# Kernel optimization log

Hardware: AMD Instinct MI355X
Metric: run time of the kernel (lower is better)

## Reference

```python
import jax, jax.numpy as jnp
import numpy as np

N = 50000      # num nodes
E = 800000     # num edges (no self loops; added in reference like add_remaining_self_loops)
D = 64         # input_dim
H = 128        # hidden_dim
O = 32         # output_dim
EPS = 1.0      # epsilon (privacy)
ALPHA = 0.5
DELTA = 1.0


def setup_inputs() -> dict:
    key = jax.random.key(0)
    ks = jax.random.split(key, 8)
    x = jax.random.normal(ks[0], (N, D), dtype=jnp.float32)
    row = jax.random.randint(ks[1], (E,), 0, N, dtype=jnp.int32)
    off = jax.random.randint(ks[2], (E,), 1, N, dtype=jnp.int32)
    col = (row + off) % N  # guarantees row != col (no pre-existing self loops)
    edge_index = jnp.stack([row, col], axis=0)
    priv_mask = jax.random.bernoulli(ks[3], 0.5, (N,))
    W1 = jax.random.normal(ks[4], (D, H), dtype=jnp.float32) * (1.0 / np.sqrt(D))
    b1 = jnp.zeros((H,), dtype=jnp.float32)
    W2 = jax.random.normal(ks[5], (H, O), dtype=jnp.float32) * (1.0 / np.sqrt(H))
    b2 = jnp.zeros((O,), dtype=jnp.float32)
    return {"x": x, "edge_index": edge_index, "priv_mask": priv_mask,
            "W1": W1, "b1": b1, "W2": W2, "b2": b2}


def _gcn_norm(edge_index, num_nodes, dtype):
    # add_remaining_self_loops + symmetric normalization deg^-1/2[row]*deg^-1/2[col]
    loops = jnp.arange(num_nodes, dtype=edge_index.dtype)
    row = jnp.concatenate([edge_index[0], loops])
    col = jnp.concatenate([edge_index[1], loops])
    deg = jax.ops.segment_sum(jnp.ones(row.shape[0], dtype=dtype), row,
                              num_segments=num_nodes)
    dis = deg ** -0.5  # deg >= 1 thanks to self loops
    norm = dis[row] * dis[col]  # [E+N]
    return row, col, norm


def reference(x, edge_index, priv_mask, W1, b1, W2, b2):
    row, col, norm = _gcn_norm(edge_index, N, x.dtype)
    exp_eps = float(np.exp(EPS))

    # ---- conv1 (GConvDP with per-node bool priv_mask) ----
    x_j = x[row]                                   # [E+N, D] gather
    p = priv_mask[row].astype(x.dtype)[:, None]    # [E+N, 1]
    transformed = ((exp_eps + 1.0) * x_j - 1.0) * (DELTA / (exp_eps - 1.0)) + ALPHA
    msg = norm[:, None] * (p * transformed + (1.0 - p) * x_j)
    h = jax.ops.segment_sum(msg, col, num_segments=N)  # scatter-add aggregate

    h = jax.nn.relu(h @ W1 + b1)
    # F.dropout skipped: reference is deterministic (eval mode)

    # ---- conv2 (called with priv_mask=False, a Python scalar) ----
    # Literal torch semantics: p_j = False -> False*(...) = 0, ~False = -1,
    # so msg = norm * (-x_j).
    msg2 = -norm[:, None] * h[row]                 # [E+N, H]
    h2 = jax.ops.segment_sum(msg2, col, num_segments=N)

    return h2 @ W2 + b2
```

## Files before the change

### kernel.cpp

```cpp
#include <hip/hip_runtime.h>
#include <math.h>

#define C1 2.163953413738653f
#define C0 -0.081976706869326f


typedef __attribute__((ext_vector_type(8))) short bf16x8;
typedef __attribute__((ext_vector_type(4))) float f32x4;

static __device__ __forceinline__ unsigned short f2bf(float f) {
    unsigned b = __float_as_uint(f);
    return (unsigned short)((b + 0x7FFFu + ((b >> 16) & 1u)) >> 16);
}
static __device__ __forceinline__ float bf2f(unsigned short u) {
    return __uint_as_float((unsigned)u << 16);
}

__global__ __launch_bounds__(1024) void k_hist2(const int* __restrict__ row,
                                                const int* __restrict__ col, int E, int chunk,
                                                int* __restrict__ hist,
                                                const float* __restrict__ W1,
                                                const float* __restrict__ W2,
                                                unsigned short* __restrict__ W1b,
                                                unsigned short* __restrict__ W2b) {
    __shared__ int hc[256], hr[256];
    int t = threadIdx.x, b = blockIdx.x;
    if (t < 256) { hc[t] = 0; hr[t] = 0; }
    __syncthreads();
    int lo = b * chunk, hi = min(E, lo + chunk);
    int base = lo + t * 4;
    for (; base + 3 < hi; base += 4096) {
        int4 r4 = *(const int4*)&row[base];
        int4 c4 = *(const int4*)&col[base];
        atomicAdd(&hc[c4.x >> 8], 1); atomicAdd(&hc[c4.y >> 8], 1);
        atomicAdd(&hc[c4.z >> 8], 1); atomicAdd(&hc[c4.w >> 8], 1);
        atomicAdd(&hr[r4.x >> 8], 1); atomicAdd(&hr[r4.y >> 8], 1);
        atomicAdd(&hr[r4.z >> 8], 1); atomicAdd(&hr[r4.w >> 8], 1);
    }
    for (; base < hi; ++base) {
        atomicAdd(&hc[col[base] >> 8], 1);
        atomicAdd(&hr[row[base] >> 8], 1);
    }
    __syncthreads();
    if (t < 256) {
        hist[t * 256 + b] = hc[t];
        hist[65536 + t * 256 + b] = hr[t];
    }
    if (b == 0) {
        for (int i = t; i < 8192; i += 1024) {
            int j = i & 7, l2 = (i >> 3) & 63, kt = (i >> 9) & 1, nt = i >> 10;
            int k = kt * 32 + (l2 >> 4) * 8 + j, n = nt * 16 + (l2 & 15);
            W1b[i] = f2bf(W1[k * 128 + n]);
        }
    } else if (b == 1) {
        for (int i = t; i < 4096; i += 1024) {
            int j = i & 7, l2 = (i >> 3) & 63, kt = (i >> 9) & 3, nt = i >> 11;
            int k = kt * 32 + (l2 >> 4) * 8 + j, n = nt * 16 + (l2 & 15);
            W2b[i] = f2bf(W2[k * 32 + n]);
        }
    }
}

__global__ void k_scan_a(const int* __restrict__ cnt, int* __restrict__ excl,
                         int* __restrict__ bsum, int n) {
    __shared__ int s[256];
    int idx = blockIdx.x * 256 + threadIdx.x;
    int v = (idx < n) ? cnt[idx] : 0;
    s[threadIdx.x] = v;
    __syncthreads();
    for (int off = 1; off < 256; off <<= 1) {
        int t = (threadIdx.x >= off) ? s[threadIdx.x - off] : 0;
        __syncthreads();
        s[threadIdx.x] += t;
        __syncthreads();
    }
    if (idx < n) excl[idx] = s[threadIdx.x] - v;
    if (threadIdx.x == 255) bsum[blockIdx.x] = s[255];
}

__global__ __launch_bounds__(1024) void k_part(const int* __restrict__ row,
                                               const int* __restrict__ col, int E, int chunk,
                                               const int* __restrict__ excl,
                                               const int* __restrict__ bsum,
                                               unsigned* __restrict__ cbuf,
                                               unsigned short* __restrict__ rbuf) {
    __shared__ int sc[512];
    __shared__ int offc[256], offr[256];
    int t = threadIdx.x, b = blockIdx.x;
    if (t < 512) sc[t] = bsum[t];
    __syncthreads();
    int half = t >> 8, d = t & 255;
    for (int off = 1; off < 256; off <<= 1) {
        int u = (t < 512 && d >= off) ? sc[half * 256 + d - off] : 0;
        __syncthreads();
        if (t < 512) sc[t] += u;
        __syncthreads();
    }
    if (t < 256) offc[t] = sc[t] - bsum[t] + excl[t * 256 + b];
    else if (t < 512) offr[d] = sc[t] - bsum[t] + excl[65536 + d * 256 + b];
    __syncthreads();
    int lo = b * chunk, hi = min(E, lo + chunk);
    int base = lo + t * 4;
    for (; base + 3 < hi; base += 4096) {
        int4 r4 = *(const int4*)&row[base];
        int4 c4 = *(const int4*)&col[base];
        int p0 = atomicAdd(&offc[c4.x >> 8], 1);
        cbuf[p0] = ((unsigned)c4.x << 16) | (unsigned)r4.x;
        int p1 = atomicAdd(&offc[c4.y >> 8], 1);
        cbuf[p1] = ((unsigned)c4.y << 16) | (unsigned)r4.y;
        int p2 = atomicAdd(&offc[c4.z >> 8], 1);
        cbuf[p2] = ((unsigned)c4.z << 16) | (unsigned)r4.z;
        int p3 = atomicAdd(&offc[c4.w >> 8], 1);
        cbuf[p3] = ((unsigned)c4.w << 16) | (unsigned)r4.w;
        int q0 = atomicAdd(&offr[r4.x >> 8], 1); rbuf[q0] = (unsigned short)r4.x;
        int q1 = atomicAdd(&offr[r4.y >> 8], 1); rbuf[q1] = (unsigned short)r4.y;
        int q2 = atomicAdd(&offr[r4.z >> 8], 1); rbuf[q2] = (unsigned short)r4.z;
        int q3 = atomicAdd(&offr[r4.w >> 8], 1); rbuf[q3] = (unsigned short)r4.w;
    }
    for (; base < hi; ++base) {
        int r = row[base], c = col[base];
        int pc = atomicAdd(&offc[c >> 8], 1);
        cbuf[pc] = ((unsigned)c << 16) | (unsigned)r;
        int pr = atomicAdd(&offr[r >> 8], 1);
        rbuf[pr] = (unsigned short)r;
    }
}

__global__ __launch_bounds__(256) void k_build(const unsigned short* __restrict__ rbuf,
                                               const unsigned* __restrict__ cbuf,
                                               const int* __restrict__ bsum,
                                               const int* __restrict__ priv,
                                               const float* __restrict__ x, int N, int E, int nbk,
                                               float* __restrict__ dis,
                                               unsigned short* __restrict__ xt,
                                               int* __restrict__ cntC, int* __restrict__ colStart,
                                               unsigned short* __restrict__ eSrc) {
    __shared__ int s1[256], s2[256], s3[256];
    int t = threadIdx.x;
    if ((int)blockIdx.x < nbk) {
        int b = blockIdx.x;
        s1[t] = (t < b) ? bsum[256 + t] : 0;
        __syncthreads();
        for (int off = 128; off > 0; off >>= 1) {
            if (t < off) s1[t] += s1[t + off];
            __syncthreads();
        }
        int rs = s1[0];
        int re = rs + bsum[256 + b];
        __syncthreads();
        s1[t] = 0;
        __syncthreads();
        for (int i = rs + t; i < re; i += 256) atomicAdd(&s1[rbuf[i] & 255], 1);
        __syncthreads();
        int node = b * 256 + t;
        float dv = rsqrtf((float)(s1[t] + 1));
        if (node < N) {
            dis[node] = dv;
            s2[t] = __float_as_int(dv);
            s3[t] = priv[node];
        } else { s2[t] = 0; s3[t] = 0; }
        __syncthreads();
        int base = b * 256;
        for (int i = t; i < 256 * 16; i += 256) {
            int ln = i >> 4;
            int n2 = base + ln;
            if (n2 >= N) continue;
            float d2 = __int_as_float(s2[ln]);
            int p = s3[ln];
            float4 v = ((const float4*)x)[(size_t)n2 * 16 + (i & 15)];
            float4 tr;
            tr.x = p ? fmaf(C1, v.x, C0) : v.x;
            tr.y = p ? fmaf(C1, v.y, C0) : v.y;
            tr.z = p ? fmaf(C1, v.z, C0) : v.z;
            tr.w = p ? fmaf(C1, v.w, C0) : v.w;
            ushort4 o;
            o.x = f2bf(d2 * tr.x); o.y = f2bf(d2 * tr.y);
            o.z = f2bf(d2 * tr.z); o.w = f2bf(d2 * tr.w);
            ((ushort4*)xt)[(size_t)n2 * 16 + (i & 15)] = o;
        }
    } else {
        int b = blockIdx.x - nbk;
        s1[t] = (t < b) ? bsum[t] : 0;
        __syncthreads();
        for (int off = 128; off > 0; off >>= 1) {
            if (t < off) s1[t] += s1[t + off];
            __syncthreads();
        }
        int cs = s1[0];
        int ce = cs + bsum[b];
        __syncthreads();
        s1[t] = 0; s3[t] = 0;
        __syncthreads();
        for (int i = cs + t; i < ce; i += 256) atomicAdd(&s1[(cbuf[i] >> 16) & 255], 1);
        __syncthreads();
        int v = s1[t];
        s2[t] = v;
        __syncthreads();
        for (int off = 1; off < 256; off <<= 1) {
            int u = (t >= off) ? s2[t - off] : 0;
            __syncthreads();
            s2[t] += u;
            __syncthreads();
        }
        int excl = s2[t] - v;
        int c = b * 256 + t;
        if (c < N) { cntC[c] = v; colStart[c] = cs + excl; }
        __syncthreads();
        s2[t] = excl;
        __syncthreads();
        for (int i = cs + t; i < ce; i += 256) {
            unsigned e = cbuf[i];
            int d = (e >> 16) & 255;
            int pos = cs + s2[d] + atomicAdd(&s3[d], 1);
            eSrc[pos] = (unsigned short)(e & 0xFFFFu);
        }
    }
}

__global__ __launch_bounds__(256) void k_gather1(const unsigned short* __restrict__ xt,
                                                 const unsigned short* __restrict__ eSrc,
                                                 const int* __restrict__ colStart,
                                                 const int* __restrict__ cntC,
                                                 const float* __restrict__ dis,
                                                 unsigned short* __restrict__ agg1b, int N) {
    int t = blockIdx.x * blockDim.x + threadIdx.x;
    int c = t >> 6, d = t & 63;
    if (c >= N) return;
    float s = bf2f(xt[(size_t)c * 64 + d]);
    int start = colStart[c], cnt = cntC[c];
    for (int base = 0; base < cnt; base += 64) {
        int m = min(cnt - base, 64);
        int ids = (d < m) ? (int)eSrc[start + base + d] : 0;
        int k = 0;
        for (; k + 8 <= m; k += 8) {
            int r0 = __shfl(ids, k),     r1 = __shfl(ids, k + 1);
            int r2 = __shfl(ids, k + 2), r3 = __shfl(ids, k + 3);
            int r4 = __shfl(ids, k + 4), r5 = __shfl(ids, k + 5);
            int r6 = __shfl(ids, k + 6), r7 = __shfl(ids, k + 7);
            float x0 = bf2f(xt[(size_t)r0 * 64 + d]);
            float x1 = bf2f(xt[(size_t)r1 * 64 + d]);
            float x2 = bf2f(xt[(size_t)r2 * 64 + d]);
            float x3 = bf2f(xt[(size_t)r3 * 64 + d]);
            float x4 = bf2f(xt[(size_t)r4 * 64 + d]);
            float x5 = bf2f(xt[(size_t)r5 * 64 + d]);
            float x6 = bf2f(xt[(size_t)r6 * 64 + d]);
            float x7 = bf2f(xt[(size_t)r7 * 64 + d]);
            s += x0; s += x1; s += x2; s += x3;
            s += x4; s += x5; s += x6; s += x7;
        }
        for (; k + 4 <= m; k += 4) {
            int r0 = __shfl(ids, k),     r1 = __shfl(ids, k + 1);
            int r2 = __shfl(ids, k + 2), r3 = __shfl(ids, k + 3);
            float x0 = bf2f(xt[(size_t)r0 * 64 + d]);
            float x1 = bf2f(xt[(size_t)r1 * 64 + d]);
            float x2 = bf2f(xt[(size_t)r2 * 64 + d]);
            float x3 = bf2f(xt[(size_t)r3 * 64 + d]);
            s += x0; s += x1; s += x2; s += x3;
        }
        for (; k < m; ++k) {
            int r = __shfl(ids, k);
            s += bf2f(xt[(size_t)r * 64 + d]);
        }
    }
    agg1b[(size_t)c * 64 + d] = f2bf(dis[c] * s);
}

__global__ __launch_bounds__(256) void k_mlp_mfma(const unsigned short* __restrict__ agg1b,
                                                  const unsigned short* __restrict__ W1b,
                                                  const float* __restrict__ b1,
                                                  const unsigned short* __restrict__ W2b,
                                                  const float* __restrict__ dis,
                                                  unsigned short* __restrict__ hps, int N) {
    __shared__ unsigned short hidA[4][16 * 136];
    const int t = threadIdx.x;
    const int w = t >> 6, l = t & 63;
    const int q = l >> 4, lm = l & 15;
    const int rowbase = blockIdx.x * 64 + w * 16;

    bf16x8 a0, a1;
    {
        int node = rowbase + lm;
        if (node >= N) node = N - 1;
        const bf16x8* pa = (const bf16x8*)(agg1b + (size_t)node * 64);
        a0 = pa[q];
        a1 = pa[4 + q];
    }
    float dvals[4];
    #pragma unroll
    for (int r = 0; r < 4; ++r) {
        int node = rowbase + q * 4 + r;
        dvals[r] = (node < N) ? dis[node] : 0.f;
    }

    const bf16x8* w1f = (const bf16x8*)W1b;
    #pragma unroll
    for (int nt = 0; nt < 8; ++nt) {
        float bv = b1[nt * 16 + lm];
        f32x4 acc = {bv, bv, bv, bv};
        acc = __builtin_amdgcn_mfma_f32_16x16x32_bf16(a0, w1f[(nt * 2 + 0) * 64 + l], acc, 0, 0, 0);
        acc = __builtin_amdgcn_mfma_f32_16x16x32_bf16(a1, w1f[(nt * 2 + 1) * 64 + l], acc, 0, 0, 0);
        #pragma unroll
        for (int r = 0; r < 4; ++r)
            hidA[w][(q * 4 + r) * 136 + nt * 16 + lm] = f2bf(fmaxf(acc[r], 0.f));
    }
    __syncthreads();

    bf16x8 ha[4];
    #pragma unroll
    for (int kt = 0; kt < 4; ++kt)
        ha[kt] = *(const bf16x8*)&hidA[w][lm * 136 + kt * 32 + q * 8];

    const bf16x8* w2f = (const bf16x8*)W2b;
    #pragma unroll
    for (int nt = 0; nt < 2; ++nt) {
        f32x4 acc = {0.f, 0.f, 0.f, 0.f};
        #pragma unroll
        for (int kt = 0; kt < 4; ++kt)
            acc = __builtin_amdgcn_mfma_f32_16x16x32_bf16(ha[kt], w2f[(nt * 4 + kt) * 64 + l], acc, 0, 0, 0);
        #pragma unroll
        for (int r = 0; r < 4; ++r) {
            int node = rowbase + q * 4 + r;
            if (node < N)
                hps[(size_t)node * 32 + nt * 16 + lm] = f2bf(acc[r] * dvals[r]);
        }
    }
}

__global__ __launch_bounds__(256) void k_gather2(const unsigned short* __restrict__ hps,
                                                 const unsigned short* __restrict__ eSrc,
                                                 const int* __restrict__ colStart,
                                                 const int* __restrict__ cntC,
                                                 const float* __restrict__ dis,
                                                 const float* __restrict__ b2,
                                                 float* __restrict__ out, int N) {
    int t = blockIdx.x * blockDim.x + threadIdx.x;
    int c = t >> 5, j = t & 31;
    if (c >= N) return;
    float s = bf2f(hps[(size_t)c * 32 + j]);
    int start = colStart[c], cnt = cntC[c];
    for (int base = 0; base < cnt; base += 32) {
        int m = min(cnt - base, 32);
        int ids = (j < m) ? (int)eSrc[start + base + j] : 0;
        int k = 0;
        for (; k + 8 <= m; k += 8) {
            int r0 = __shfl(ids, k, 32),     r1 = __shfl(ids, k + 1, 32);
            int r2 = __shfl(ids, k + 2, 32), r3 = __shfl(ids, k + 3, 32);
            int r4 = __shfl(ids, k + 4, 32), r5 = __shfl(ids, k + 5, 32);
            int r6 = __shfl(ids, k + 6, 32), r7 = __shfl(ids, k + 7, 32);
            float h0 = bf2f(hps[(size_t)r0 * 32 + j]);
            float h1 = bf2f(hps[(size_t)r1 * 32 + j]);
            float h2 = bf2f(hps[(size_t)r2 * 32 + j]);
            float h3 = bf2f(hps[(size_t)r3 * 32 + j]);
            float h4 = bf2f(hps[(size_t)r4 * 32 + j]);
            float h5 = bf2f(hps[(size_t)r5 * 32 + j]);
            float h6 = bf2f(hps[(size_t)r6 * 32 + j]);
            float h7 = bf2f(hps[(size_t)r7 * 32 + j]);
            s += h0; s += h1; s += h2; s += h3;
            s += h4; s += h5; s += h6; s += h7;
        }
        for (; k + 4 <= m; k += 4) {
            int r0 = __shfl(ids, k, 32),     r1 = __shfl(ids, k + 1, 32);
            int r2 = __shfl(ids, k + 2, 32), r3 = __shfl(ids, k + 3, 32);
            float h0 = bf2f(hps[(size_t)r0 * 32 + j]);
            float h1 = bf2f(hps[(size_t)r1 * 32 + j]);
            float h2 = bf2f(hps[(size_t)r2 * 32 + j]);
            float h3 = bf2f(hps[(size_t)r3 * 32 + j]);
            s += h0; s += h1; s += h2; s += h3;
        }
        for (; k < m; ++k) {
            int r = __shfl(ids, k, 32);
            s += bf2f(hps[(size_t)r * 32 + j]);
        }
    }
    out[(size_t)c * 32 + j] = b2[j] - dis[c] * s;
}

extern "C" void kernel_launch(void* const* d_in, const int* in_sizes, int n_in,
                              void* d_out, int out_size, void* d_ws, size_t ws_size,
                              hipStream_t stream) {
    const float* x    = (const float*)d_in[0];
    const int*   ei   = (const int*)d_in[1];
    const int*   priv = (const int*)d_in[2];
    const float* W1   = (const float*)d_in[3];
    const float* b1   = (const float*)d_in[4];
    const float* W2   = (const float*)d_in[5];
    const float* b2   = (const float*)d_in[6];
    float* out = (float*)d_out;

    const int N = in_sizes[2];
    const int E = in_sizes[1] / 2;
    const int* row = ei;
    const int* col = ei + E;

    char* ws = (char*)d_ws;
    size_t off = 0;
    auto take = [&](size_t bytes) { char* p = ws + off; off = (off + bytes + 255) & ~(size_t)255; return p; };
    int*            hist     = (int*)           take((size_t)131072 * 4);
    int*            excl     = (int*)           take((size_t)131072 * 4);
    int*            bsum     = (int*)           take(512 * 4);
    unsigned short* W1b      = (unsigned short*)take((size_t)8192 * 2);
    unsigned short* W2b      = (unsigned short*)take((size_t)4096 * 2);
    unsigned*       cbuf     = (unsigned*)      take((size_t)E * 4);
    unsigned short* rbuf     = (unsigned short*)take((size_t)E * 2);
    float*          dis      = (float*)         take((size_t)N * 4);
    int*            cntC     = (int*)           take((size_t)N * 4);
    int*            colStart = (int*)           take((size_t)N * 4);
    unsigned short* eSrc     = (unsigned short*)take((size_t)E * 2);
    unsigned short* xt       = (unsigned short*)take((size_t)N * 64 * 2);
    unsigned short* agg1b    = (unsigned short*)take((size_t)N * 64 * 2);
    unsigned short* hps      = (unsigned short*)take((size_t)N * 32 * 2);
    (void)ws_size;

    const int chunk = (((E + 255) / 256) + 3) & ~3;
    const int nbk = (N + 255) / 256;

    k_hist2   <<<256, 1024, 0, stream>>>(row, col, E, chunk, hist, W1, W2, W1b, W2b);
    k_scan_a  <<<512, 256, 0, stream>>>(hist, excl, bsum, 131072);
    k_part    <<<256, 1024, 0, stream>>>(row, col, E, chunk, excl, bsum, cbuf, rbuf);
    k_build   <<<2 * nbk, 256, 0, stream>>>(rbuf, cbuf, bsum, priv, x, N, E, nbk,
                                            dis, xt, cntC, colStart, eSrc);
    k_gather1 <<<((size_t)N * 64 + 255) / 256, 256, 0, stream>>>(xt, eSrc, colStart, cntC, dis, agg1b, N);
    k_mlp_mfma<<<(N + 63) / 64, 256, 0, stream>>>(agg1b, W1b, b1, W2b, dis, hps, N);
    k_gather2 <<<((size_t)N * 32 + 255) / 256, 256, 0, stream>>>(hps, eSrc, colStart, cntC, dis, b2, out, N);
}
```

Baseline: 155.9 us.

## Split layer-1 feature table into column halves and gather each half separately

Stores the scaled bf16 input features as two separate 32-column tables and runs the first neighbour-sum gather twice, once per half. Each wavefront now serves two nodes at 32 lanes each. The intent is to shrink the randomly accessed working set per pass (3.2 MB per half) so it fits better in L2/LLC and improves hit rate. The cost is reading the edge lists twice, an extra launch, and 64-byte row segments per gather instead of 128-byte ones.

Measured after the change: 162.2 us. 1.04x slower.

```diff
diff --git a/kernel.cpp b/kernel.cpp
--- a/kernel.cpp
+++ b/kernel.cpp
@@ -132,7 +132,8 @@
                                                const int* __restrict__ priv,
                                                const float* __restrict__ x, int N, int E, int nbk,
                                                float* __restrict__ dis,
-                                               unsigned short* __restrict__ xt,
+                                               unsigned short* __restrict__ xtL,
+                                               unsigned short* __restrict__ xtH,
                                                int* __restrict__ cntC, int* __restrict__ colStart,
                                                unsigned short* __restrict__ eSrc) {
     __shared__ int s1[256], s2[256], s3[256];
@@ -162,12 +163,12 @@
         __syncthreads();
         int base = b * 256;
         for (int i = t; i < 256 * 16; i += 256) {
-            int ln = i >> 4;
+            int ln = i >> 4, q = i & 15;
             int n2 = base + ln;
             if (n2 >= N) continue;
             float d2 = __int_as_float(s2[ln]);
             int p = s3[ln];
-            float4 v = ((const float4*)x)[(size_t)n2 * 16 + (i & 15)];
+            float4 v = ((const float4*)x)[(size_t)n2 * 16 + q];
             float4 tr;
             tr.x = p ? fmaf(C1, v.x, C0) : v.x;
             tr.y = p ? fmaf(C1, v.y, C0) : v.y;
@@ -176,7 +177,8 @@
             ushort4 o;
             o.x = f2bf(d2 * tr.x); o.y = f2bf(d2 * tr.y);
             o.z = f2bf(d2 * tr.z); o.w = f2bf(d2 * tr.w);
-            ((ushort4*)xt)[(size_t)n2 * 16 + (i & 15)] = o;
+            if (q < 8) ((ushort4*)xtL)[(size_t)n2 * 8 + q] = o;
+            else       ((ushort4*)xtH)[(size_t)n2 * 8 + (q - 8)] = o;
         }
     } else {
         int b = blockIdx.x - nbk;
@@ -217,52 +219,56 @@
     }
 }
 
-__global__ __launch_bounds__(256) void k_gather1(const unsigned short* __restrict__ xt,
-                                                 const unsigned short* __restrict__ eSrc,
-                                                 const int* __restrict__ colStart,
-                                                 const int* __restrict__ cntC,
-                                                 const float* __restrict__ dis,
-                                                 unsigned short* __restrict__ agg1b, int N) {
+__global__ __launch_bounds__(256) void k_gather1_half(const unsigned short* __restrict__ xth,
+                                                      const unsigned short* __restrict__ eSrc,
+                                                      const int* __restrict__ colStart,
+                                                      const int* __restrict__ cntC,
+                                                      const float* __restrict__ dis,
+                                                      unsigned short* __restrict__ agg1b,
+                                                      int N, int halfOff) {
     int t = blockIdx.x * blockDim.x + threadIdx.x;
-    int c = t >> 6, d = t & 63;
-    if (c >= N) return;
-    float s = bf2f(xt[(size_t)c * 64 + d]);
+    int Nh = (N + 1) >> 1;
+    int wid = t >> 6, l = t & 63;
+    int lane = l & 31, hf = l >> 5;
+    int c = wid + hf * Nh;
+    if (wid >= Nh || c >= N) return;
+    float s = bf2f(xth[(size_t)c * 32 + lane]);
     int start = colStart[c], cnt = cntC[c];
-    for (int base = 0; base < cnt; base += 64) {
-        int m = min(cnt - base, 64);
-        int ids = (d < m) ? (int)eSrc[start + base + d] : 0;
+    for (int base = 0; base < cnt; base += 32) {
+        int m = min(cnt - base, 32);
+        int ids = (lane < m) ? (int)eSrc[start + base + lane] : 0;
         int k = 0;
         for (; k + 8 <= m; k += 8) {
-            int r0 = __shfl(ids, k),     r1 = __shfl(ids, k + 1);
-            int r2 = __shfl(ids, k + 2), r3 = __shfl(ids, k + 3);
-            int r4 = __shfl(ids, k + 4), r5 = __shfl(ids, k + 5);
-            int r6 = __shfl(ids, k + 6), r7 = __shfl(ids, k + 7);
-            float x0 = bf2f(xt[(size_t)r0 * 64 + d]);
-            float x1 = bf2f(xt[(size_t)r1 * 64 + d]);
-            float x2 = bf2f(xt[(size_t)r2 * 64 + d]);
-            float x3 = bf2f(xt[(size_t)r3 * 64 + d]);
-            float x4 = bf2f(xt[(size_t)r4 * 64 + d]);
-            float x5 = bf2f(xt[(size_t)r5 * 64 + d]);
-            float x6 = bf2f(xt[(size_t)r6 * 64 + d]);
-            float x7 = bf2f(xt[(size_t)r7 * 64 + d]);
+            int r0 = __shfl(ids, k, 32),     r1 = __shfl(ids, k + 1, 32);
+            int r2 = __shfl(ids, k + 2, 32), r3 = __shfl(ids, k + 3, 32);
+            int r4 = __shfl(ids, k + 4, 32), r5 = __shfl(ids, k + 5, 32);
+            int r6 = __shfl(ids, k + 6, 32), r7 = __shfl(ids, k + 7, 32);
+            float x0 = bf2f(xth[(size_t)r0 * 32 + lane]);
+            float x1 = bf2f(xth[(size_t)r1 * 32 + lane]);
+            float x2 = bf2f(xth[(size_t)r2 * 32 + lane]);
+            float x3 = bf2f(xth[(size_t)r3 * 32 + lane]);
+            float x4 = bf2f(xth[(size_t)r4 * 32 + lane]);
+            float x5 = bf2f(xth[(size_t)r5 * 32 + lane]);
+            float x6 = bf2f(xth[(size_t)r6 * 32 + lane]);
+            float x7 = bf2f(xth[(size_t)r7 * 32 + lane]);
             s += x0; s += x1; s += x2; s += x3;
             s += x4; s += x5; s += x6; s += x7;
         }
         for (; k + 4 <= m; k += 4) {
-            int r0 = __shfl(ids, k),     r1 = __shfl(ids, k + 1);
-            int r2 = __shfl(ids, k + 2), r3 = __shfl(ids, k + 3);
-            float x0 = bf2f(xt[(size_t)r0 * 64 + d]);
-            float x1 = bf2f(xt[(size_t)r1 * 64 + d]);
-            float x2 = bf2f(xt[(size_t)r2 * 64 + d]);
-            float x3 = bf2f(xt[(size_t)r3 * 64 + d]);
+            int r0 = __shfl(ids, k, 32),     r1 = __shfl(ids, k + 1, 32);
+            int r2 = __shfl(ids, k + 2, 32), r3 = __shfl(ids, k + 3, 32);
+            float x0 = bf2f(xth[(size_t)r0 * 32 + lane]);
+            float x1 = bf2f(xth[(size_t)r1 * 32 + lane]);
+            float x2 = bf2f(xth[(size_t)r2 * 32 + lane]);
+            float x3 = bf2f(xth[(size_t)r3 * 32 + lane]);
             s += x0; s += x1; s += x2; s += x3;
         }
         for (; k < m; ++k) {
-            int r = __shfl(ids, k);
-            s += bf2f(xt[(size_t)r * 64 + d]);
-        }
-    }
-    agg1b[(size_t)c * 64 + d] = f2bf(dis[c] * s);
+            int r = __shfl(ids, k, 32);
+            s += bf2f(xth[(size_t)r * 32 + lane]);
+        }
+    }
+    agg1b[(size_t)c * 64 + halfOff + lane] = f2bf(dis[c] * s);
 }
 
 __global__ __launch_bounds__(256) void k_mlp_mfma(const unsigned short* __restrict__ agg1b,
@@ -406,20 +412,24 @@
     int*            cntC     = (int*)           take((size_t)N * 4);
     int*            colStart = (int*)           take((size_t)N * 4);
     unsigned short* eSrc     = (unsigned short*)take((size_t)E * 2);
-    unsigned short* xt       = (unsigned short*)take((size_t)N * 64 * 2);
+    unsigned short* xtL      = (unsigned short*)take((size_t)N * 32 * 2);
+    unsigned short* xtH      = (unsigned short*)take((size_t)N * 32 * 2);
     unsigned short* agg1b    = (unsigned short*)take((size_t)N * 64 * 2);
     unsigned short* hps      = (unsigned short*)take((size_t)N * 32 * 2);
     (void)ws_size;
 
     const int chunk = (((E + 255) / 256) + 3) & ~3;
     const int nbk = (N + 255) / 256;
+    const int Nh = (N + 1) / 2;
+    const int gblocks = (int)(((size_t)Nh * 64 + 255) / 256);
 
     k_hist2   <<<256, 1024, 0, stream>>>(row, col, E, chunk, hist, W1, W2, W1b, W2b);
     k_scan_a  <<<512, 256, 0, stream>>>(hist, excl, bsum, 131072);
     k_part    <<<256, 1024, 0, stream>>>(row, col, E, chunk, excl, bsum, cbuf, rbuf);
     k_build   <<<2 * nbk, 256, 0, stream>>>(rbuf, cbuf, bsum, priv, x, N, E, nbk,
-                                            dis, xt, cntC, colStart, eSrc);
-    k_gather1 <<<((size_t)N * 64 + 255) / 256, 256, 0, stream>>>(xt, eSrc, colStart, cntC, dis, agg1b, N);
+                                            dis, xtL, xtH, cntC, colStart, eSrc);
+    k_gather1_half<<<gblocks, 256, 0, stream>>>(xtL, eSrc, colStart, cntC, dis, agg1b, N, 0);
+    k_gather1_half<<<gblocks, 256, 0, stream>>>(xtH, eSrc, colStart, cntC, dis, agg1b, N, 32);
     k_mlp_mfma<<<(N + 63) / 64, 256, 0, stream>>>(agg1b, W1b, b1, W2b, dis, hps, N);
     k_gather2 <<<((size_t)N * 32 + 255) / 256, 256, 0, stream>>>(hps, eSrc, colStart, cntC, dis, b2, out, N);
 }
```
